# Kernel optimization log

Measured on AMD Instinct MI355X. Metric: run time of the kernel, lower is better.

## Reference

```python
import jax, jax.numpy as jnp
import numpy as np

N_NODES = 100000
N_EDGES = 1600000
IN_CH = 128
HID = 64


def gcn_conv(x, W, b, src, dst, n):
    """PyG-style GCNConv: add self-loops, symmetric deg^-1/2 normalization."""
    h = x @ W  # [n, out]
    # degree including self-loop, computed from destination (col) indices
    deg = jax.ops.segment_sum(jnp.ones_like(dst, dtype=h.dtype), dst, num_segments=n) + 1.0
    dinv = jax.lax.rsqrt(deg)  # [n]
    norm = dinv[src] * dinv[dst]  # [E]
    agg = jax.ops.segment_sum(h[src] * norm[:, None], dst, num_segments=n)
    agg = agg + h * (1.0 / deg)[:, None]  # self-loop term: norm = 1/deg
    return agg + b


def setup_inputs() -> dict:
    key = jax.random.key(0)
    ks = jax.random.split(key, 6)
    x = jax.random.normal(ks[0], (N_NODES, IN_CH), dtype=jnp.float32)
    edge_index = jax.random.randint(ks[1], (2, N_EDGES), 0, N_NODES, dtype=jnp.int64)
    W1 = jax.random.normal(ks[2], (IN_CH, HID), dtype=jnp.float32) / np.sqrt(IN_CH)
    b1 = jnp.zeros((HID,), dtype=jnp.float32)
    W2 = jax.random.normal(ks[3], (HID, HID), dtype=jnp.float32) / np.sqrt(HID)
    b2 = jnp.zeros((HID,), dtype=jnp.float32)
    Wl = jax.random.normal(ks[4], (HID, 1), dtype=jnp.float32) / np.sqrt(HID)
    bl = jnp.zeros((1,), dtype=jnp.float32)
    return {"x": x, "edge_index": edge_index, "W1": W1, "b1": b1,
            "W2": W2, "b2": b2, "Wl": Wl, "bl": bl}


def reference(x, edge_index, W1, b1, W2, b2, Wl, bl):
    src, dst = edge_index[0], edge_index[1]
    n = x.shape[0]
    h = gcn_conv(x, W1, b1, src, dst, n)
    h = jax.nn.relu(h)
    # dropout: identity in eval mode
    h = gcn_conv(h, W2, b2, src, dst, n)
    h = jax.nn.relu(h)
    out = (h @ Wl + bl)[:, 0]  # [n]
    return out
```

## Files before the change

### kernel.cpp

```cpp
#include <hip/hip_runtime.h>
#include <hip/hip_fp16.h>


#define SHIFT 9
#define BSZ   (1 << SHIFT)
#define NBMAX 256
#define BIN_CH 2048
#define BCAP  12288

using f16x8 = __attribute__((ext_vector_type(8))) _Float16;
using f16x2 = __attribute__((ext_vector_type(2))) _Float16;
using f32x4 = __attribute__((ext_vector_type(4))) float;

__global__ __launch_bounds__(256) void k_bin(const int* __restrict__ src,
                                             const int* __restrict__ dst,
                                             int* __restrict__ bcursor,
                                             unsigned* __restrict__ binned,
                                             __half* __restrict__ hs, int n, int E) {
    if (blockIdx.x == 0 && threadIdx.x < 8) {
        uint4 z = {0u, 0u, 0u, 0u};
        reinterpret_cast<uint4*>(hs + ((size_t)n << 6))[threadIdx.x] = z;
    }
    __shared__ int h[NBMAX];
    __shared__ int base[NBMAX];
    const int beg = blockIdx.x * BIN_CH;
    const int end = min(beg + BIN_CH, E);
    for (int i = threadIdx.x; i < NBMAX; i += 256) h[i] = 0;
    __syncthreads();
    for (int e = beg + threadIdx.x; e < end; e += 256)
        atomicAdd(&h[dst[e] >> SHIFT], 1);
    __syncthreads();
    for (int i = threadIdx.x; i < NBMAX; i += 256) {
        base[i] = h[i] ? atomicAdd(&bcursor[i], h[i]) : 0;
        h[i] = 0;
    }
    __syncthreads();
    for (int e = beg + threadIdx.x; e < end; e += 256) {
        int d = dst[e];
        int b = d >> SHIFT;
        int off = atomicAdd(&h[b], 1);
        binned[(size_t)b * BCAP + base[b] + off] =
            (unsigned)src[e] | ((unsigned)(d & (BSZ - 1)) << 17);
    }
}

__global__ __launch_bounds__(256) void k_bfill(const unsigned* __restrict__ binned,
                                               const int* __restrict__ counts,
                                               int* __restrict__ rowptr,
                                               int* __restrict__ colidx,
                                               float* __restrict__ dinv, int n) {
    __shared__ int cnt[BSZ];
    __shared__ int nbase[BSZ];
    __shared__ int stmp[256];
    const int b = blockIdx.x;
    const int t = threadIdx.x;
    stmp[t] = (t < b) ? counts[t] : 0;
    __syncthreads();
    for (int off = 128; off; off >>= 1) {
        if (t < off) stmp[t] += stmp[t + off];
        __syncthreads();
    }
    const int ebeg = stmp[0];
    const int ecnt = counts[b];
    __syncthreads();
    const unsigned* bp = binned + (size_t)b * BCAP;
    for (int i = t; i < BSZ; i += 256) cnt[i] = 0;
    __syncthreads();
    for (int e = t; e < ecnt; e += 256)
        atomicAdd(&cnt[bp[e] >> 17], 1);
    __syncthreads();
    int c0 = cnt[2 * t], c1 = cnt[2 * t + 1];
    int s = c0 + c1;
    stmp[t] = s;
    __syncthreads();
    for (int off = 1; off < 256; off <<= 1) {
        int u = (t >= off) ? stmp[t - off] : 0;
        __syncthreads();
        stmp[t] += u;
        __syncthreads();
    }
    int ex = stmp[t] - s;
    nbase[2 * t] = ex;
    nbase[2 * t + 1] = ex + c0;
    __syncthreads();
    const int gbase = b << SHIFT;
    for (int j = t; j < BSZ; j += 256) {
        int g = gbase + j;
        if (g < n) {
            rowptr[g] = (int)(((unsigned)(ebeg + nbase[j]) << 8) |
                              (unsigned)min(cnt[j], 255));
            dinv[g] = rsqrtf((float)cnt[j] + 1.0f);
        }
        cnt[j] = nbase[j];
    }
    __syncthreads();
    for (int e = t; e < ecnt; e += 256) {
        unsigned p = bp[e];
        int j = p >> 17;
        int off = atomicAdd(&cnt[j], 1);
        colidx[ebeg + off] = (int)((p & 0x1FFFFu) << 7);
    }
}

template <int K, bool A_FP32>
__global__ __launch_bounds__(256) void k_gemm_mfma(const void* __restrict__ Av,
                                                   const float* __restrict__ W,
                                                   const float* __restrict__ dinv,
                                                   __half* __restrict__ C, int n) {
    constexpr int KP = K + 8;
    __shared__ _Float16 Wt[64 * KP];
    const int tid = threadIdx.x;
    for (int i = tid; i < K * 64; i += 256) {
        int k = i >> 6, c = i & 63;
        Wt[c * KP + k] = (_Float16)W[i];
    }
    __syncthreads();

    const int lane = tid & 63;
    const int wv = tid >> 6;
    const int r16 = lane & 15;
    const int kq = lane >> 4;
    const int rb = blockIdx.x * 64 + wv * 16;
    const int arow = min(rb + r16, n - 1);

    f32x4 acc[4] = {{0.f,0.f,0.f,0.f},{0.f,0.f,0.f,0.f},
                    {0.f,0.f,0.f,0.f},{0.f,0.f,0.f,0.f}};

#pragma unroll
    for (int kk = 0; kk < K; kk += 32) {
        f16x8 a;
        if (A_FP32) {
            const float* Ap = (const float*)Av + (size_t)arow * K + kk + kq * 8;
            float4 f0 = *reinterpret_cast<const float4*>(Ap);
            float4 f1 = *reinterpret_cast<const float4*>(Ap + 4);
            a[0] = (_Float16)f0.x; a[1] = (_Float16)f0.y;
            a[2] = (_Float16)f0.z; a[3] = (_Float16)f0.w;
            a[4] = (_Float16)f1.x; a[5] = (_Float16)f1.y;
            a[6] = (_Float16)f1.z; a[7] = (_Float16)f1.w;
        } else {
            const _Float16* Ap = (const _Float16*)Av + (size_t)arow * K + kk + kq * 8;
            a = *reinterpret_cast<const f16x8*>(Ap);
        }
#pragma unroll
        for (int nt = 0; nt < 4; ++nt) {
            f16x8 b = *reinterpret_cast<const f16x8*>(&Wt[(nt * 16 + r16) * KP + kk + kq * 8]);
            acc[nt] = __builtin_amdgcn_mfma_f32_16x16x32_f16(a, b, acc[nt], 0, 0, 0);
        }
    }

#pragma unroll
    for (int r = 0; r < 4; ++r) {
        const int row = rb + kq * 4 + r;
        if (row < n) {
            const float di = dinv[row];
#pragma unroll
            for (int nt = 0; nt < 4; ++nt)
                C[((size_t)row << 6) + nt * 16 + r16] = __float2half(acc[nt][r] * di);
        }
    }
}

__device__ __forceinline__ void dotu4(float acc[8], uint4 u, f16x2 pl, f16x2 ph) {
    union { uint4 u4; f16x2 h[4]; } v;
    v.u4 = u;
    acc[0] = __builtin_amdgcn_fdot2(v.h[0], pl, acc[0], false);
    acc[1] = __builtin_amdgcn_fdot2(v.h[0], ph, acc[1], false);
    acc[2] = __builtin_amdgcn_fdot2(v.h[1], pl, acc[2], false);
    acc[3] = __builtin_amdgcn_fdot2(v.h[1], ph, acc[3], false);
    acc[4] = __builtin_amdgcn_fdot2(v.h[2], pl, acc[4], false);
    acc[5] = __builtin_amdgcn_fdot2(v.h[2], ph, acc[5], false);
    acc[6] = __builtin_amdgcn_fdot2(v.h[3], pl, acc[6], false);
    acc[7] = __builtin_amdgcn_fdot2(v.h[3], ph, acc[7], false);
}

__device__ __forceinline__ void fold8(float acc[8]) {
#pragma unroll
    for (int m = 8; m <= 32; m <<= 1) {
#pragma unroll
        for (int j = 0; j < 8; ++j)
            acc[j] += __shfl_xor(acc[j], m, 64);
    }
}

__device__ __forceinline__ void gather_pair(const char* __restrict__ hsb,
                                            const int* __restrict__ colidx,
                                            unsigned pk0, unsigned pk1,
                                            int g, int p, unsigned dum,
                                            float acc0[8], float acc1[8]) {
    const f16x2 pl = {(_Float16)1.0f, (_Float16)0.0f};
    const f16x2 ph = {(_Float16)0.0f, (_Float16)1.0f};
    const int beg0 = (int)(pk0 >> 8), deg0 = (int)(pk0 & 255u);
    const int beg1 = (int)(pk1 >> 8), deg1 = (int)(pk1 & 255u);
    const int t0 = deg0 - g, t1 = deg1 - g;
    const unsigned poff = (unsigned)(p << 4);
    const unsigned dumo = dum + poff;
    const int ia = beg0 + g;
    const int ib = beg1 + g;
    unsigned a0 = (unsigned)colidx[ia]      + poff;
    unsigned a1 = (unsigned)colidx[ia + 8]  + poff;
    unsigned a2 = (unsigned)colidx[ia + 16] + poff;
    unsigned a3 = (unsigned)colidx[ia + 24] + poff;
    unsigned b0 = (unsigned)colidx[ib]      + poff;
    unsigned b1 = (unsigned)colidx[ib + 8]  + poff;
    unsigned b2 = (unsigned)colidx[ib + 16] + poff;
    unsigned b3 = (unsigned)colidx[ib + 24] + poff;
    unsigned oa0 = (0  < t0) ? a0 : dumo;
    unsigned oa1 = (8  < t0) ? a1 : dumo;
    unsigned oa2 = (16 < t0) ? a2 : dumo;
    unsigned oa3 = (24 < t0) ? a3 : dumo;
    unsigned ob0 = (0  < t1) ? b0 : dumo;
    unsigned ob1 = (8  < t1) ? b1 : dumo;
    unsigned ob2 = (16 < t1) ? b2 : dumo;
    unsigned ob3 = (24 < t1) ? b3 : dumo;
    uint4 ua0 = *reinterpret_cast<const uint4*>(hsb + oa0);
    uint4 ua1 = *reinterpret_cast<const uint4*>(hsb + oa1);
    uint4 ua2 = *reinterpret_cast<const uint4*>(hsb + oa2);
    uint4 ua3 = *reinterpret_cast<const uint4*>(hsb + oa3);
    uint4 ub0 = *reinterpret_cast<const uint4*>(hsb + ob0);
    uint4 ub1 = *reinterpret_cast<const uint4*>(hsb + ob1);
    uint4 ub2 = *reinterpret_cast<const uint4*>(hsb + ob2);
    uint4 ub3 = *reinterpret_cast<const uint4*>(hsb + ob3);
    dotu4(acc0, ua0, pl, ph);
    dotu4(acc0, ua1, pl, ph);
    dotu4(acc0, ua2, pl, ph);
    dotu4(acc0, ua3, pl, ph);
    dotu4(acc1, ub0, pl, ph);
    dotu4(acc1, ub1, pl, ph);
    dotu4(acc1, ub2, pl, ph);
    dotu4(acc1, ub3, pl, ph);
    const int ns0 = (deg0 + 7) >> 3;
    for (int k = 4; k < ns0; k += 4) {
        const int ik = beg0 + 8 * k + g;
        unsigned c0 = (unsigned)colidx[ik]      + poff;
        unsigned c1 = (unsigned)colidx[ik + 8]  + poff;
        unsigned c2 = (unsigned)colidx[ik + 16] + poff;
        unsigned c3 = (unsigned)colidx[ik + 24] + poff;
        const int kb = 8 * k;
        uint4 u0 = *reinterpret_cast<const uint4*>(hsb + ((kb      < t0) ? c0 : dumo));
        uint4 u1 = *reinterpret_cast<const uint4*>(hsb + ((kb + 8  < t0) ? c1 : dumo));
        uint4 u2 = *reinterpret_cast<const uint4*>(hsb + ((kb + 16 < t0) ? c2 : dumo));
        uint4 u3 = *reinterpret_cast<const uint4*>(hsb + ((kb + 24 < t0) ? c3 : dumo));
        dotu4(acc0, u0, pl, ph);
        dotu4(acc0, u1, pl, ph);
        dotu4(acc0, u2, pl, ph);
        dotu4(acc0, u3, pl, ph);
    }
    const int ns1 = (deg1 + 7) >> 3;
    for (int k = 4; k < ns1; k += 4) {
        const int ik = beg1 + 8 * k + g;
        unsigned c0 = (unsigned)colidx[ik]      + poff;
        unsigned c1 = (unsigned)colidx[ik + 8]  + poff;
        unsigned c2 = (unsigned)colidx[ik + 16] + poff;
        unsigned c3 = (unsigned)colidx[ik + 24] + poff;
        const int kb = 8 * k;
        uint4 u0 = *reinterpret_cast<const uint4*>(hsb + ((kb      < t1) ? c0 : dumo));
        uint4 u1 = *reinterpret_cast<const uint4*>(hsb + ((kb + 8  < t1) ? c1 : dumo));
        uint4 u2 = *reinterpret_cast<const uint4*>(hsb + ((kb + 16 < t1) ? c2 : dumo));
        uint4 u3 = *reinterpret_cast<const uint4*>(hsb + ((kb + 24 < t1) ? c3 : dumo));
        dotu4(acc1, u0, pl, ph);
        dotu4(acc1, u1, pl, ph);
        dotu4(acc1, u2, pl, ph);
        dotu4(acc1, u3, pl, ph);
    }
    fold8(acc0);
    fold8(acc1);
}

__global__ __launch_bounds__(256) void k_agg_relu(const __half* __restrict__ hs,
                                                  const int* __restrict__ rowptr,
                                                  const int* __restrict__ colidx,
                                                  const float* __restrict__ dinv,
                                                  const float* __restrict__ b,
                                                  __half* __restrict__ out, int n) {
    const int wv = threadIdx.x >> 6;
    const int i0 = blockIdx.x * 8 + wv * 2;
    const int lane = threadIdx.x & 63;
    if (i0 >= n) return;
    const int i1 = min(i0 + 1, n - 1);
    const int g = lane >> 3, p = lane & 7;
    const int iw = (lane & 8) ? i1 : i0;
    const unsigned pk0 = (unsigned)rowptr[i0];
    const unsigned pk1 = (unsigned)rowptr[i1];
    uint4 su = *reinterpret_cast<const uint4*>(hs + ((size_t)iw << 6) + (p << 3));
    const float di = dinv[iw];
    float acc0[8] = {}, acc1[8] = {};
    gather_pair((const char*)hs, colidx, pk0, pk1, g, p, (unsigned)n << 7,
                acc0, acc1);
    if (lane < 16) {
        const f16x2 pl = {(_Float16)1.0f, (_Float16)0.0f};
        const f16x2 ph = {(_Float16)0.0f, (_Float16)1.0f};
        float a[8];
#pragma unroll
        for (int j = 0; j < 8; ++j) a[j] = (lane & 8) ? acc1[j] : acc0[j];
        dotu4(a, su, pl, ph);
        float4 b0 = *reinterpret_cast<const float4*>(b + (p << 3));
        float4 b1 = *reinterpret_cast<const float4*>(b + (p << 3) + 4);
        __half2 h0 = __halves2half2(__float2half(fmaxf(fmaf(a[0], di, b0.x), 0.f)),
                                    __float2half(fmaxf(fmaf(a[1], di, b0.y), 0.f)));
        __half2 h1 = __halves2half2(__float2half(fmaxf(fmaf(a[2], di, b0.z), 0.f)),
                                    __float2half(fmaxf(fmaf(a[3], di, b0.w), 0.f)));
        __half2 h2 = __halves2half2(__float2half(fmaxf(fmaf(a[4], di, b1.x), 0.f)),
                                    __float2half(fmaxf(fmaf(a[5], di, b1.y), 0.f)));
        __half2 h3 = __halves2half2(__float2half(fmaxf(fmaf(a[6], di, b1.z), 0.f)),
                                    __float2half(fmaxf(fmaf(a[7], di, b1.w), 0.f)));
        uint4 u;
        u.x = *reinterpret_cast<unsigned*>(&h0);
        u.y = *reinterpret_cast<unsigned*>(&h1);
        u.z = *reinterpret_cast<unsigned*>(&h2);
        u.w = *reinterpret_cast<unsigned*>(&h3);
        if (iw < n && (i0 + 1 < n || !(lane & 8)))
            *reinterpret_cast<uint4*>(out + ((size_t)iw << 6) + (p << 3)) = u;
    }
}

__global__ __launch_bounds__(256) void k_agg_head(const __half* __restrict__ hs,
                                                  const int* __restrict__ rowptr,
                                                  const int* __restrict__ colidx,
                                                  const float* __restrict__ dinv,
                                                  const float* __restrict__ b2,
                                                  const float* __restrict__ Wl,
                                                  const float* __restrict__ bl,
                                                  float* __restrict__ out, int n) {
    const int wv = threadIdx.x >> 6;
    const int i0 = blockIdx.x * 8 + wv * 2;
    const int lane = threadIdx.x & 63;
    if (i0 >= n) return;
    const int i1 = min(i0 + 1, n - 1);
    const int g = lane >> 3, p = lane & 7;
    const int iw = (lane & 8) ? i1 : i0;
    const unsigned pk0 = (unsigned)rowptr[i0];
    const unsigned pk1 = (unsigned)rowptr[i1];
    uint4 su = *reinterpret_cast<const uint4*>(hs + ((size_t)iw << 6) + (p << 3));
    const float di = dinv[iw];
    float acc0[8] = {}, acc1[8] = {};
    gather_pair((const char*)hs, colidx, pk0, pk1, g, p, (unsigned)n << 7,
                acc0, acc1);
    const f16x2 pl = {(_Float16)1.0f, (_Float16)0.0f};
    const f16x2 ph = {(_Float16)0.0f, (_Float16)1.0f};
    float a[8];
#pragma unroll
    for (int j = 0; j < 8; ++j) a[j] = (lane & 8) ? acc1[j] : acc0[j];
    dotu4(a, su, pl, ph);
    float4 b0 = *reinterpret_cast<const float4*>(b2 + (p << 3));
    float4 b1 = *reinterpret_cast<const float4*>(b2 + (p << 3) + 4);
    float4 w0 = *reinterpret_cast<const float4*>(Wl + (p << 3));
    float4 w1 = *reinterpret_cast<const float4*>(Wl + (p << 3) + 4);
    float v = fmaxf(fmaf(a[0], di, b0.x), 0.f) * w0.x
            + fmaxf(fmaf(a[1], di, b0.y), 0.f) * w0.y
            + fmaxf(fmaf(a[2], di, b0.z), 0.f) * w0.z
            + fmaxf(fmaf(a[3], di, b0.w), 0.f) * w0.w
            + fmaxf(fmaf(a[4], di, b1.x), 0.f) * w1.x
            + fmaxf(fmaf(a[5], di, b1.y), 0.f) * w1.y
            + fmaxf(fmaf(a[6], di, b1.z), 0.f) * w1.z
            + fmaxf(fmaf(a[7], di, b1.w), 0.f) * w1.w;
    v += __shfl_xor(v, 1, 64);
    v += __shfl_xor(v, 2, 64);
    v += __shfl_xor(v, 4, 64);
    if (lane == 0) out[i0] = v + bl[0];
    if (lane == 8 && i0 + 1 < n) out[i1] = v + bl[0];
}

extern "C" void kernel_launch(void* const* d_in, const int* in_sizes, int n_in,
                              void* d_out, int out_size, void* d_ws, size_t ws_size,
                              hipStream_t stream) {
    const float* x  = (const float*)d_in[0];
    const int*   ei = (const int*)d_in[1];
    const float* W1 = (const float*)d_in[2];
    const float* b1 = (const float*)d_in[3];
    const float* W2 = (const float*)d_in[4];
    const float* b2 = (const float*)d_in[5];
    const float* Wl = (const float*)d_in[6];
    const float* bl = (const float*)d_in[7];
    float* out = (float*)d_out;

    const int n = in_sizes[0] / 128;
    const int E = in_sizes[1] / 2;
    const int* src = ei;
    const int* dst = ei + E;
    const int nb = (n + BSZ - 1) >> SHIFT;

    char* ws = (char*)d_ws;
    size_t o = 0;
    auto alloc = [&](size_t bytes) {
        void* p = ws + o;
        o = (o + bytes + 255) & ~(size_t)255;
        return p;
    };
    float* dinv    = (float*)alloc((size_t)n * 4);
    int*   bcursor = (int*)  alloc((size_t)NBMAX * 4);
    int*   rowptr  = (int*)  alloc((size_t)(n + 1) * 4);
    int*   colidx  = (int*)  alloc(((size_t)E + 64) * 4);
    __half* hs     = (__half*)alloc((size_t)(n + 1) * 64 * 2);
    __half* bufA   = (__half*)alloc((size_t)n * 64 * 2);
    unsigned* binned = (unsigned*)alloc((size_t)nb * BCAP * 4);

    hipMemsetAsync(bcursor, 0, NBMAX * sizeof(int), stream);
    k_bin<<<(E + BIN_CH - 1) / BIN_CH, 256, 0, stream>>>(src, dst, bcursor, binned,
                                                         hs, n, E);
    k_bfill<<<nb, 256, 0, stream>>>(binned, bcursor, rowptr, colidx, dinv, n);

    k_gemm_mfma<128, true><<<(n + 63) / 64, 256, 0, stream>>>(x, W1, dinv, hs, n);
    k_agg_relu<<<(n + 7) / 8, 256, 0, stream>>>(hs, rowptr, colidx, dinv, b1, bufA, n);

    k_gemm_mfma<64, false><<<(n + 63) / 64, 256, 0, stream>>>(bufA, W2, dinv, hs, n);
    k_agg_head<<<(n + 7) / 8, 256, 0, stream>>>(hs, rowptr, colidx, dinv, b2, Wl, bl,
                                                out, n);
}
```

Before: 148.7 us.

## Shrink dst bins and privatize LDS histograms per wavefront in binning kernels

Halves the destination bin size to 256 nodes, which doubles the number of bins and halves the per-block edge chunk and bin capacity. Binning and fill kernels now keep one LDS histogram per wavefront, so atomic contention on shared counters drops. Per-wave offsets come from a small per-bin prefix over the four waves, and in the fill kernel each thread now owns exactly one node. The risk is twice as many k_bin blocks and global bcursor atomics, plus a halved bin capacity that could overflow with skewed degree distributions.

```diff
diff --git a/kernel.cpp b/kernel.cpp
--- a/kernel.cpp
+++ b/kernel.cpp
@@ -2,11 +2,11 @@
 #include <hip/hip_fp16.h>
 
 
-#define SHIFT 9
+#define SHIFT 8
 #define BSZ   (1 << SHIFT)
-#define NBMAX 256
-#define BIN_CH 2048
-#define BCAP  12288
+#define NBMAX 512
+#define BIN_CH 1024
+#define BCAP  6144
 
 using f16x8 = __attribute__((ext_vector_type(8))) _Float16;
 using f16x2 = __attribute__((ext_vector_type(2))) _Float16;
@@ -21,25 +21,31 @@
         uint4 z = {0u, 0u, 0u, 0u};
         reinterpret_cast<uint4*>(hs + ((size_t)n << 6))[threadIdx.x] = z;
     }
-    __shared__ int h[NBMAX];
-    __shared__ int base[NBMAX];
+    __shared__ int h[4][NBMAX];
+    const int t = threadIdx.x;
+    const int wv = t >> 6;
     const int beg = blockIdx.x * BIN_CH;
     const int end = min(beg + BIN_CH, E);
-    for (int i = threadIdx.x; i < NBMAX; i += 256) h[i] = 0;
-    __syncthreads();
-    for (int e = beg + threadIdx.x; e < end; e += 256)
-        atomicAdd(&h[dst[e] >> SHIFT], 1);
-    __syncthreads();
-    for (int i = threadIdx.x; i < NBMAX; i += 256) {
-        base[i] = h[i] ? atomicAdd(&bcursor[i], h[i]) : 0;
-        h[i] = 0;
-    }
-    __syncthreads();
-    for (int e = beg + threadIdx.x; e < end; e += 256) {
+    for (int i = t; i < 4 * NBMAX; i += 256) (&h[0][0])[i] = 0;
+    __syncthreads();
+    for (int e = beg + t; e < end; e += 256)
+        atomicAdd(&h[wv][dst[e] >> SHIFT], 1);
+    __syncthreads();
+    for (int i = t; i < NBMAX; i += 256) {
+        int c0 = h[0][i], c1 = h[1][i], c2 = h[2][i], c3 = h[3][i];
+        int tot = c0 + c1 + c2 + c3;
+        int gb = tot ? atomicAdd(&bcursor[i], tot) : 0;
+        h[0][i] = gb;
+        h[1][i] = gb + c0;
+        h[2][i] = gb + c0 + c1;
+        h[3][i] = gb + c0 + c1 + c2;
+    }
+    __syncthreads();
+    for (int e = beg + t; e < end; e += 256) {
         int d = dst[e];
         int b = d >> SHIFT;
-        int off = atomicAdd(&h[b], 1);
-        binned[(size_t)b * BCAP + base[b] + off] =
+        int off = atomicAdd(&h[wv][b], 1);
+        binned[(size_t)b * BCAP + off] =
             (unsigned)src[e] | ((unsigned)(d & (BSZ - 1)) << 17);
     }
 }
@@ -49,12 +55,14 @@
                                                int* __restrict__ rowptr,
                                                int* __restrict__ colidx,
                                                float* __restrict__ dinv, int n) {
-    __shared__ int cnt[BSZ];
-    __shared__ int nbase[BSZ];
+    __shared__ int c[4][BSZ];
     __shared__ int stmp[256];
     const int b = blockIdx.x;
     const int t = threadIdx.x;
-    stmp[t] = (t < b) ? counts[t] : 0;
+    const int wv = t >> 6;
+    int s0 = 0;
+    for (int j = t; j < b; j += 256) s0 += counts[j];
+    stmp[t] = s0;
     __syncthreads();
     for (int off = 128; off; off >>= 1) {
         if (t < off) stmp[t] += stmp[t + off];
@@ -64,13 +72,13 @@
     const int ecnt = counts[b];
     __syncthreads();
     const unsigned* bp = binned + (size_t)b * BCAP;
-    for (int i = t; i < BSZ; i += 256) cnt[i] = 0;
+    for (int i = t; i < 4 * BSZ; i += 256) (&c[0][0])[i] = 0;
     __syncthreads();
     for (int e = t; e < ecnt; e += 256)
-        atomicAdd(&cnt[bp[e] >> 17], 1);
-    __syncthreads();
-    int c0 = cnt[2 * t], c1 = cnt[2 * t + 1];
-    int s = c0 + c1;
+        atomicAdd(&c[wv][bp[e] >> 17], 1);
+    __syncthreads();
+    int c0 = c[0][t], c1 = c[1][t], c2 = c[2][t], c3 = c[3][t];
+    int s = c0 + c1 + c2 + c3;
     stmp[t] = s;
     __syncthreads();
     for (int off = 1; off < 256; off <<= 1) {
@@ -79,25 +87,21 @@
         stmp[t] += u;
         __syncthreads();
     }
-    int ex = stmp[t] - s;
-    nbase[2 * t] = ex;
-    nbase[2 * t + 1] = ex + c0;
-    __syncthreads();
-    const int gbase = b << SHIFT;
-    for (int j = t; j < BSZ; j += 256) {
-        int g = gbase + j;
-        if (g < n) {
-            rowptr[g] = (int)(((unsigned)(ebeg + nbase[j]) << 8) |
-                              (unsigned)min(cnt[j], 255));
-            dinv[g] = rsqrtf((float)cnt[j] + 1.0f);
-        }
-        cnt[j] = nbase[j];
-    }
+    const int ex = stmp[t] - s;
+    const int g = (b << SHIFT) + t;
+    if (g < n) {
+        rowptr[g] = (int)(((unsigned)(ebeg + ex) << 8) | (unsigned)min(s, 255));
+        dinv[g] = rsqrtf((float)s + 1.0f);
+    }
+    c[0][t] = ex;
+    c[1][t] = ex + c0;
+    c[2][t] = ex + c0 + c1;
+    c[3][t] = ex + c0 + c1 + c2;
     __syncthreads();
     for (int e = t; e < ecnt; e += 256) {
         unsigned p = bp[e];
         int j = p >> 17;
-        int off = atomicAdd(&cnt[j], 1);
+        int off = atomicAdd(&c[wv][j], 1);
         colidx[ebeg + off] = (int)((p & 0x1FFFFu) << 7);
     }
 }
```

Result: slower. 166.6 us (+12.1%).

## Replace global atomic bucket cursors with per-block local binning and offset table

Applied to the files above, without the earlier changes.

The edge-binning pass no longer reserves space in global per-bucket buckets through global atomics. Each block now sorts its 1024-edge chunk locally by destination bucket, using vectorized int4 loads, and writes a per-block prefix table of bucket offsets. The fill kernel walks that table to gather each bucket's segments into a shared-memory position map, then counts and scatters as before. This drops the global atomics and the memset, but adds a serial per-block gather loop in k_bfill, scattered reads, and a large shared array that can lower occupancy.

```diff
diff --git a/kernel.cpp b/kernel.cpp
--- a/kernel.cpp
+++ b/kernel.cpp
@@ -5,8 +5,8 @@
 #define SHIFT 9
 #define BSZ   (1 << SHIFT)
 #define NBMAX 256
-#define BIN_CH 2048
-#define BCAP  12288
+#define BIN_CH 1024
+#define PMAX  12288
 
 using f16x8 = __attribute__((ext_vector_type(8))) _Float16;
 using f16x2 = __attribute__((ext_vector_type(2))) _Float16;
@@ -14,64 +14,36 @@
 
 __global__ __launch_bounds__(256) void k_bin(const int* __restrict__ src,
                                              const int* __restrict__ dst,
-                                             int* __restrict__ bcursor,
                                              unsigned* __restrict__ binned,
-                                             __half* __restrict__ hs, int n, int E) {
+                                             int* __restrict__ gbase,
+                                             __half* __restrict__ hs,
+                                             int n, int nb, int E) {
     if (blockIdx.x == 0 && threadIdx.x < 8) {
         uint4 z = {0u, 0u, 0u, 0u};
         reinterpret_cast<uint4*>(hs + ((size_t)n << 6))[threadIdx.x] = z;
     }
     __shared__ int h[NBMAX];
-    __shared__ int base[NBMAX];
-    const int beg = blockIdx.x * BIN_CH;
-    const int end = min(beg + BIN_CH, E);
-    for (int i = threadIdx.x; i < NBMAX; i += 256) h[i] = 0;
-    __syncthreads();
-    for (int e = beg + threadIdx.x; e < end; e += 256)
-        atomicAdd(&h[dst[e] >> SHIFT], 1);
-    __syncthreads();
-    for (int i = threadIdx.x; i < NBMAX; i += 256) {
-        base[i] = h[i] ? atomicAdd(&bcursor[i], h[i]) : 0;
-        h[i] = 0;
-    }
-    __syncthreads();
-    for (int e = beg + threadIdx.x; e < end; e += 256) {
-        int d = dst[e];
-        int b = d >> SHIFT;
-        int off = atomicAdd(&h[b], 1);
-        binned[(size_t)b * BCAP + base[b] + off] =
-            (unsigned)src[e] | ((unsigned)(d & (BSZ - 1)) << 17);
-    }
-}
-
-__global__ __launch_bounds__(256) void k_bfill(const unsigned* __restrict__ binned,
-                                               const int* __restrict__ counts,
-                                               int* __restrict__ rowptr,
-                                               int* __restrict__ colidx,
-                                               float* __restrict__ dinv, int n) {
-    __shared__ int cnt[BSZ];
-    __shared__ int nbase[BSZ];
+    __shared__ int ex[NBMAX + 1];
+    __shared__ int cur[NBMAX];
     __shared__ int stmp[256];
-    const int b = blockIdx.x;
     const int t = threadIdx.x;
-    stmp[t] = (t < b) ? counts[t] : 0;
-    __syncthreads();
-    for (int off = 128; off; off >>= 1) {
-        if (t < off) stmp[t] += stmp[t + off];
-        __syncthreads();
-    }
-    const int ebeg = stmp[0];
-    const int ecnt = counts[b];
-    __syncthreads();
-    const unsigned* bp = binned + (size_t)b * BCAP;
-    for (int i = t; i < BSZ; i += 256) cnt[i] = 0;
-    __syncthreads();
-    for (int e = t; e < ecnt; e += 256)
-        atomicAdd(&cnt[bp[e] >> 17], 1);
-    __syncthreads();
-    int c0 = cnt[2 * t], c1 = cnt[2 * t + 1];
-    int s = c0 + c1;
-    stmp[t] = s;
+    const int blk = blockIdx.x;
+    const int beg = blk * BIN_CH;
+    for (int i = t; i < NBMAX; i += 256) h[i] = 0;
+    __syncthreads();
+    const int e4 = beg + t * 4;
+    const bool act = e4 < E;
+    int4 d4 = {0, 0, 0, 0};
+    if (act) {
+        d4 = *reinterpret_cast<const int4*>(dst + e4);
+        atomicAdd(&h[d4.x >> SHIFT], 1);
+        atomicAdd(&h[d4.y >> SHIFT], 1);
+        atomicAdd(&h[d4.z >> SHIFT], 1);
+        atomicAdd(&h[d4.w >> SHIFT], 1);
+    }
+    __syncthreads();
+    const int hv = (t < nb) ? h[t] : 0;
+    stmp[t] = hv;
     __syncthreads();
     for (int off = 1; off < 256; off <<= 1) {
         int u = (t >= off) ? stmp[t - off] : 0;
@@ -79,13 +51,85 @@
         stmp[t] += u;
         __syncthreads();
     }
-    int ex = stmp[t] - s;
+    if (t <= nb) ex[t] = stmp[t] - ((t < nb) ? h[t] : 0);
+    __syncthreads();
+    if (t < nb) cur[t] = ex[t];
+    if (t <= nb) gbase[(size_t)blk * (nb + 1) + t] = ex[t];
+    __syncthreads();
+    if (act) {
+        const int4 s4 = *reinterpret_cast<const int4*>(src + e4);
+        int b0 = d4.x >> SHIFT, b1 = d4.y >> SHIFT;
+        int b2 = d4.z >> SHIFT, b3 = d4.w >> SHIFT;
+        int p0 = atomicAdd(&cur[b0], 1);
+        int p1 = atomicAdd(&cur[b1], 1);
+        int p2 = atomicAdd(&cur[b2], 1);
+        int p3 = atomicAdd(&cur[b3], 1);
+        binned[beg + p0] = (unsigned)s4.x | ((unsigned)(d4.x & (BSZ - 1)) << 17);
+        binned[beg + p1] = (unsigned)s4.y | ((unsigned)(d4.y & (BSZ - 1)) << 17);
+        binned[beg + p2] = (unsigned)s4.z | ((unsigned)(d4.z & (BSZ - 1)) << 17);
+        binned[beg + p3] = (unsigned)s4.w | ((unsigned)(d4.w & (BSZ - 1)) << 17);
+    }
+}
+
+__global__ __launch_bounds__(256) void k_bfill(const unsigned* __restrict__ binned,
+                                               const int* __restrict__ gbase,
+                                               int nblk, int nb,
+                                               int* __restrict__ rowptr,
+                                               int* __restrict__ colidx,
+                                               float* __restrict__ dinv, int n) {
+    __shared__ int posmap[PMAX];
+    __shared__ int cnt[BSZ];
+    __shared__ int nbase[BSZ];
+    __shared__ int stmp[256];
+    __shared__ int sh_tot;
+    const int b = blockIdx.x;
+    const int t = threadIdx.x;
+    if (t == 0) sh_tot = 0;
+    for (int i = t; i < BSZ; i += 256) cnt[i] = 0;
+    __syncthreads();
+    int ebeg_part = 0;
+    for (int blk = t; blk < nblk; blk += 256) {
+        const int* gb = gbase + (size_t)blk * (nb + 1) + b;
+        const int s0 = gb[0];
+        const int s1 = gb[1];
+        ebeg_part += s0;
+        const int c = s1 - s0;
+        if (c > 0) {
+            int pos = atomicAdd(&sh_tot, c);
+            const int base = blk * BIN_CH + s0;
+            for (int k = 0; k < c; ++k)
+                if (pos + k < PMAX) posmap[pos + k] = base + k;
+        }
+    }
+    stmp[t] = ebeg_part;
+    __syncthreads();
+    for (int off = 128; off; off >>= 1) {
+        if (t < off) stmp[t] += stmp[t + off];
+        __syncthreads();
+    }
+    const int ebeg = stmp[0];
+    const int ecnt = min(sh_tot, PMAX);
+    __syncthreads();
+    for (int j = t; j < ecnt; j += 256)
+        atomicAdd(&cnt[binned[posmap[j]] >> 17], 1);
+    __syncthreads();
+    int c0 = cnt[2 * t], c1 = cnt[2 * t + 1];
+    int s = c0 + c1;
+    stmp[t] = s;
+    __syncthreads();
+    for (int off = 1; off < 256; off <<= 1) {
+        int u = (t >= off) ? stmp[t - off] : 0;
+        __syncthreads();
+        stmp[t] += u;
+        __syncthreads();
+    }
+    const int ex = stmp[t] - s;
     nbase[2 * t] = ex;
     nbase[2 * t + 1] = ex + c0;
     __syncthreads();
-    const int gbase = b << SHIFT;
+    const int gb9 = b << SHIFT;
     for (int j = t; j < BSZ; j += 256) {
-        int g = gbase + j;
+        const int g = gb9 + j;
         if (g < n) {
             rowptr[g] = (int)(((unsigned)(ebeg + nbase[j]) << 8) |
                               (unsigned)min(cnt[j], 255));
@@ -94,11 +138,11 @@
         cnt[j] = nbase[j];
     }
     __syncthreads();
-    for (int e = t; e < ecnt; e += 256) {
-        unsigned p = bp[e];
-        int j = p >> 17;
-        int off = atomicAdd(&cnt[j], 1);
-        colidx[ebeg + off] = (int)((p & 0x1FFFFu) << 7);
+    for (int j = t; j < ecnt; j += 256) {
+        const unsigned e = binned[posmap[j]];
+        const int lo = (int)(e >> 17);
+        const int off = atomicAdd(&cnt[lo], 1);
+        colidx[ebeg + off] = (int)((e & 0x1FFFFu) << 7);
     }
 }
 
@@ -378,6 +422,7 @@
     const int* src = ei;
     const int* dst = ei + E;
     const int nb = (n + BSZ - 1) >> SHIFT;
+    const int nblk = (E + BIN_CH - 1) / BIN_CH;
 
     char* ws = (char*)d_ws;
     size_t o = 0;
@@ -387,17 +432,16 @@
         return p;
     };
     float* dinv    = (float*)alloc((size_t)n * 4);
-    int*   bcursor = (int*)  alloc((size_t)NBMAX * 4);
     int*   rowptr  = (int*)  alloc((size_t)(n + 1) * 4);
     int*   colidx  = (int*)  alloc(((size_t)E + 64) * 4);
+    int*   gbase   = (int*)  alloc((size_t)nblk * (nb + 1) * 4);
     __half* hs     = (__half*)alloc((size_t)(n + 1) * 64 * 2);
     __half* bufA   = (__half*)alloc((size_t)n * 64 * 2);
-    unsigned* binned = (unsigned*)alloc((size_t)nb * BCAP * 4);
-
-    hipMemsetAsync(bcursor, 0, NBMAX * sizeof(int), stream);
-    k_bin<<<(E + BIN_CH - 1) / BIN_CH, 256, 0, stream>>>(src, dst, bcursor, binned,
-                                                         hs, n, E);
-    k_bfill<<<nb, 256, 0, stream>>>(binned, bcursor, rowptr, colidx, dinv, n);
+    unsigned* binned = (unsigned*)alloc(((size_t)nblk * BIN_CH) * 4);
+
+    k_bin<<<nblk, 256, 0, stream>>>(src, dst, binned, gbase, hs, n, nb, E);
+    k_bfill<<<nb, 256, 0, stream>>>(binned, gbase, nblk, nb, rowptr, colidx,
+                                    dinv, n);
 
     k_gemm_mfma<128, true><<<(n + 63) / 64, 256, 0, stream>>>(x, W1, dinv, hs, n);
     k_agg_relu<<<(n + 7) / 8, 256, 0, stream>>>(hs, rowptr, colidx, dinv, b1, bufA, n);
```

Result: slower. 153.8 us (+3.5%).
